# Optimization experiments

Measured on AMD Instinct MI355X. Metric: run time of the kernel, lower is better.

Reference implementation:

```python
import jax, jax.numpy as jnp
import numpy as np

TEMP = 0.05  # contrastive temperature (ContrastiveLoss.temp)
N, D = 8192, 128


def setup_inputs() -> dict:
    key = jax.random.key(0)
    k1, k2 = jax.random.split(key)
    x = jax.random.normal(k1, (N, D), dtype=jnp.float32)
    # Binary positive-pair label matrix; diagonal forced to 1 so every row
    # has at least one positive (positive_pair_nums > 0).
    y = (jax.random.uniform(k2, (N, N)) < 0.05).astype(jnp.float32)
    y = jnp.maximum(y, jnp.eye(N, dtype=jnp.float32))
    return {"x": x, "y": y}


def reference(x, y):
    # similarity(): L2-normalize rows, cosine matmul, exp(cos / temp)
    x_norm = x / jnp.linalg.norm(x, axis=1, keepdims=True)        # [N, D]
    cos_sim = jnp.exp(jnp.matmul(x_norm, x_norm.T) / TEMP)        # [N, N]

    positive_pair_nums = jnp.sum(y, axis=-1)                      # [N]
    neg_y = 1.0 - y
    # hard_mode == 'normal': negative mass per anchor
    nl = jnp.sum(cos_sim * neg_y, axis=-1, keepdims=True)         # [N, 1]

    # sm = log(cos_sim / (cos_sim + nl)); average over positives per row
    sm = jnp.log(cos_sim / (cos_sim + nl))                        # [N, N]
    lm = jnp.sum(sm * y, axis=-1) / positive_pair_nums            # [N]
    return -jnp.mean(lm)
```

## Files before the change

kernel.cpp:

```cpp
#include <hip/hip_runtime.h>
#include <hip/hip_bf16.h>


#define NN 8192

typedef short bf16x8 __attribute__((ext_vector_type(8)));
typedef float f32x4 __attribute__((ext_vector_type(4)));
typedef unsigned long long u64;
typedef unsigned int u32;

__device__ inline unsigned short f32_to_bf16_rne(float f) {
    unsigned u = __float_as_uint(f);
    unsigned r = 0x7FFFu + ((u >> 16) & 1u);
    return (unsigned short)((u + r) >> 16);
}

__global__ __launch_bounds__(256) void prep_kernel(
    const float* __restrict__ x, const float* __restrict__ y,
    unsigned short* __restrict__ xn, u64* __restrict__ bits,
    float* __restrict__ Pp) {
    const int t = threadIdx.x;
    const int w = t >> 6, l = t & 63;
    if (blockIdx.x < 2048) {
        const int row = blockIdx.x * 4 + w;
        float2 v = reinterpret_cast<const float2*>(x)[row * 64 + l];
        float ss = v.x * v.x + v.y * v.y;
#pragma unroll
        for (int m = 1; m < 64; m <<= 1) ss += __shfl_xor(ss, m);
        float rn = 1.0f / sqrtf(ss);
        ushort2 st;
        st.x = f32_to_bf16_rne(v.x * rn);
        st.y = f32_to_bf16_rne(v.y * rn);
        reinterpret_cast<ushort2*>(xn)[row * 64 + l] = st;
    } else {
        const int r = (blockIdx.x - 2048) * 4 + w;
        const float4* yr =
            reinterpret_cast<const float4*>(y + (size_t)r * NN);
        u64* br = bits + (size_t)r * 128;
        int pc = 0;
#pragma unroll 4
        for (int g = 0; g < 32; ++g) {
            float4 v = yr[g * 64 + l];
            u64 m0 = __ballot(v.x != 0.0f);
            u64 m1 = __ballot(v.y != 0.0f);
            u64 m2 = __ballot(v.z != 0.0f);
            u64 m3 = __ballot(v.w != 0.0f);
            pc += __popcll(m0) + __popcll(m1) + __popcll(m2) + __popcll(m3);
            if (l == 0) {
                br[g * 4 + 0] = m0;
                br[g * 4 + 1] = m1;
                br[g * 4 + 2] = m2;
                br[g * 4 + 3] = m3;
            }
        }
        if (l == 0) Pp[r] = (float)pc;
    }
}

template <bool DIAG>
__device__ __forceinline__ void epilogue(
    const f32x4 (&acc)[4][2], const u32 (&W0)[4], const u32 (&W1)[4],
    int shbase, int wM, int wN, int lm16, int lh, int l,
    float* __restrict__ Lb) {
#pragma unroll
    for (int qq = 0; qq < 2; ++qq) {
        float T = 0.0f, A = 0.0f, Y = 0.0f;
        const int rl = wN * 32 + qq * 16 + lm16;
#pragma unroll
        for (int p = 0; p < 4; ++p) {
            const int cl = wM * 64 + p * 16 + lh * 4;
#pragma unroll
            for (int j = 0; j < 4; ++j) {
                float s = 20.0f * acc[p][qq][j];
                float e = __expf(s);
                u32 word = qq ? W1[j] : W0[j];
                u32 bit = (word >> (shbase + p * 4)) & 1u;
                if (DIAG) {
                    if (cl + j == rl) {
                        e = 0.0f;
                        bit = 0u;
                    }
                }
                T += e;
                A += bit ? s : 0.0f;
                Y += bit ? e : 0.0f;
            }
        }
        T += __shfl_xor(T, 16); T += __shfl_xor(T, 32);
        A += __shfl_xor(A, 16); A += __shfl_xor(A, 32);
        Y += __shfl_xor(Y, 16); Y += __shfl_xor(Y, 32);
        if (l < 16) {
            const int r = wN * 32 + qq * 16 + l;
            Lb[(wM * 3 + 0) * 128 + r] = T;
            Lb[(wM * 3 + 1) * 128 + r] = A;
            Lb[(wM * 3 + 2) * 128 + r] = Y;
        }
    }
}

__global__ __launch_bounds__(512, 4) void contrast_main_kernel(
    const unsigned short* __restrict__ xn, const u64* __restrict__ bits,
    float* __restrict__ PtT, float* __restrict__ PtA,
    float* __restrict__ PtY) {
    __shared__ __align__(1024) char lds[68608];
    float* Lb = reinterpret_cast<float*>(lds + 65536);

    const int bid = blockIdx.x;
    const int swz = (bid & 7) * 512 + (bid >> 3);
    const int cb = swz & 63, rb = swz >> 6;
    const int t = threadIdx.x;
    const int w = t >> 6, l = t & 63;
    const int wM = w & 1, wN = w >> 1;
    const int lm16 = l & 15, lh = l >> 4;

    const int g4 = (cb >> 1) * 4;
    const int rbase = rb * 128 + wN * 32;
    u64 B0[4], B1[4];
    {
        const u64* bp0 = bits + (size_t)(rbase + lm16) * 128 + g4;
        const u64* bp1 = bits + (size_t)(rbase + 16 + lm16) * 128 + g4;
        ulonglong2 a0 = *reinterpret_cast<const ulonglong2*>(bp0);
        ulonglong2 a1 = *reinterpret_cast<const ulonglong2*>(bp0 + 2);
        ulonglong2 c0 = *reinterpret_cast<const ulonglong2*>(bp1);
        ulonglong2 c1 = *reinterpret_cast<const ulonglong2*>(bp1 + 2);
        B0[0] = a0.x; B0[1] = a0.y; B0[2] = a1.x; B0[3] = a1.y;
        B1[0] = c0.x; B1[1] = c0.y; B1[2] = c1.x; B1[3] = c1.y;
    }
    const int base = (cb & 1) * 32 + wM * 16;
    const bool hi = base >= 32;
    u32 W0[4], W1[4];
#pragma unroll
    for (int e = 0; e < 4; ++e) {
        W0[e] = hi ? (u32)(B0[e] >> 32) : (u32)B0[e];
        W1[e] = hi ? (u32)(B1[e] >> 32) : (u32)B1[e];
    }
    const int shbase = (base & 31) + lh;

    {
        const char* xb = reinterpret_cast<const char*>(xn);
        const char* srcA = xb + (size_t)cb * 32768;
        const char* srcB = xb + (size_t)rb * 32768;
#pragma unroll
        for (int i = 0; i < 8; ++i) {
            const int p = i * 8192 + t * 16;
            const int pp = p & 32767;
            const int src = pp ^ (((pp >> 8) & 7) << 4);
            __builtin_amdgcn_global_load_lds(
                (const __attribute__((address_space(1))) void*)(
                    (i < 4 ? srcA : srcB) + src),
                (__attribute__((address_space(3))) void*)(lds + p), 16, 0, 0);
        }
    }
    asm volatile("s_waitcnt vmcnt(0)" ::: "memory");
    __syncthreads();

    f32x4 acc[4][2];
#pragma unroll
    for (int i = 0; i < 4; ++i)
#pragma unroll
        for (int j = 0; j < 2; ++j) {
            f32x4 z = {0.0f, 0.0f, 0.0f, 0.0f};
            acc[i][j] = z;
        }

#pragma unroll
    for (int ks = 0; ks < 4; ++ks) {
        bf16x8 af[4], bfr[2];
#pragma unroll
        for (int p = 0; p < 4; ++p) {
            const int c = wM * 64 + p * 16 + lm16;
            const int v = c * 256 + ks * 64 + lh * 16;
            af[p] = *reinterpret_cast<const bf16x8*>(lds + (v ^ ((c & 7) << 4)));
        }
#pragma unroll
        for (int qq = 0; qq < 2; ++qq) {
            const int r = wN * 32 + qq * 16 + lm16;
            const int v = r * 256 + ks * 64 + lh * 16;
            bfr[qq] = *reinterpret_cast<const bf16x8*>(
                lds + 32768 + (v ^ ((r & 7) << 4)));
        }
#pragma unroll
        for (int p = 0; p < 4; ++p)
#pragma unroll
            for (int qq = 0; qq < 2; ++qq)
                acc[p][qq] = __builtin_amdgcn_mfma_f32_16x16x32_bf16(
                    af[p], bfr[qq], acc[p][qq], 0, 0, 0);
    }

    if (rb == cb)
        epilogue<true>(acc, W0, W1, shbase, wM, wN, lm16, lh, l, Lb);
    else
        epilogue<false>(acc, W0, W1, shbase, wM, wN, lm16, lh, l, Lb);
    __syncthreads();

    if (t < 128) {
        const size_t o = (size_t)cb * NN + rb * 128 + t;
        PtT[o] = Lb[0 * 128 + t] + Lb[3 * 128 + t];
        PtA[o] = Lb[1 * 128 + t] + Lb[4 * 128 + t];
        PtY[o] = Lb[2 * 128 + t] + Lb[5 * 128 + t];
    }
}

__global__ __launch_bounds__(256) void finalize_kernel(
    const float* __restrict__ PtT, const float* __restrict__ PtA,
    const float* __restrict__ PtY, const float* __restrict__ Pp,
    float* __restrict__ out) {
    const int t = threadIdx.x;
    const int r = blockIdx.x * 256 + t;
    float T = 0.0f, A = 0.0f, Y = 0.0f;
#pragma unroll 8
    for (int cb = 0; cb < 64; ++cb) {
        T += PtT[(size_t)cb * NN + r];
        A += PtA[(size_t)cb * NN + r];
        Y += PtY[(size_t)cb * NN + r];
    }
    const float P = Pp[r];
    const float nl = T - Y;
    const float lm =
        (A - (P - 1.0f) * logf(nl) - log1pf(nl * 2.0611536e-9f)) / P;

    __shared__ float red[256];
    red[t] = lm;
    __syncthreads();
    for (int k = 128; k > 0; k >>= 1) {
        if (t < k) red[t] += red[t + k];
        __syncthreads();
    }
    if (t == 0) atomicAdd(out, -red[0] * (1.0f / (float)NN));
}

extern "C" void kernel_launch(void* const* d_in, const int* in_sizes, int n_in,
                              void* d_out, int out_size, void* d_ws,
                              size_t ws_size, hipStream_t stream) {
    const float* x = (const float*)d_in[0];
    const float* y = (const float*)d_in[1];

    char* ws = (char*)d_ws;
    unsigned short* xn = (unsigned short*)ws;
    u64* bits = (u64*)(ws + (2ull << 20));
    float* PtT = (float*)(ws + (10ull << 20));
    float* PtA = (float*)(ws + (12ull << 20));
    float* PtY = (float*)(ws + (14ull << 20));
    float* Pp = (float*)(ws + (16ull << 20));

    hipMemsetAsync(d_out, 0, sizeof(float), stream);
    prep_kernel<<<4096, 256, 0, stream>>>(x, y, xn, bits, Pp);
    contrast_main_kernel<<<4096, 512, 0, stream>>>(xn, bits, PtT, PtA, PtY);
    finalize_kernel<<<NN / 256, 256, 0, stream>>>(PtT, PtA, PtY, Pp,
                                                  (float*)d_out);
}
```

Baseline: 410.9 us.

## Shrink main kernel tile to 64x64 with 256 threads and drop LDS reduction

Cuts the Gram-matrix tile from 128x128 (512 threads, 8 waves) to 64x64 (256 threads, 4 waves), quadrupling the grid to 16384 blocks and halving LDS per block. Each wave now owns a whole 16-row strip, so partial sums go straight to global memory and the cross-wave LDS reduction and its second barrier are removed. In exchange the partial-sum buffers double to 128 column blocks, finalize reads twice as much, and operand reuse per loaded byte falls. Also raises the unroll factor of the bit-packing loop in prep.

New measurement: 426.4 us. 3.8% more time.

```diff
diff --git a/kernel.cpp b/kernel.cpp
--- a/kernel.cpp
+++ b/kernel.cpp
@@ -38,7 +38,7 @@
             reinterpret_cast<const float4*>(y + (size_t)r * NN);
         u64* br = bits + (size_t)r * 128;
         int pc = 0;
-#pragma unroll 4
+#pragma unroll 8
         for (int g = 0; g < 32; ++g) {
             float4 v = yr[g * 64 + l];
             u64 m0 = __ballot(v.x != 0.0f);
@@ -59,146 +59,118 @@
 
 template <bool DIAG>
 __device__ __forceinline__ void epilogue(
-    const f32x4 (&acc)[4][2], const u32 (&W0)[4], const u32 (&W1)[4],
-    int shbase, int wM, int wN, int lm16, int lh, int l,
-    float* __restrict__ Lb) {
-#pragma unroll
-    for (int qq = 0; qq < 2; ++qq) {
-        float T = 0.0f, A = 0.0f, Y = 0.0f;
-        const int rl = wN * 32 + qq * 16 + lm16;
-#pragma unroll
-        for (int p = 0; p < 4; ++p) {
-            const int cl = wM * 64 + p * 16 + lh * 4;
-#pragma unroll
-            for (int j = 0; j < 4; ++j) {
-                float s = 20.0f * acc[p][qq][j];
-                float e = __expf(s);
-                u32 word = qq ? W1[j] : W0[j];
-                u32 bit = (word >> (shbase + p * 4)) & 1u;
-                if (DIAG) {
-                    if (cl + j == rl) {
-                        e = 0.0f;
-                        bit = 0u;
-                    }
+    const f32x4 (&acc)[4], const u32 (&W)[4], int shbase, int w, int lm16,
+    int lh, int l, int rb, int cb, float* __restrict__ PtT,
+    float* __restrict__ PtA, float* __restrict__ PtY) {
+    float T = 0.0f, A = 0.0f, Y = 0.0f;
+    const int rl = w * 16 + lm16;
+#pragma unroll
+    for (int p = 0; p < 4; ++p) {
+#pragma unroll
+        for (int j = 0; j < 4; ++j) {
+            float s = 20.0f * acc[p][j];
+            float e = __expf(s);
+            u32 bit = (W[j] >> (shbase + p * 4)) & 1u;
+            if (DIAG) {
+                if (p * 16 + lh * 4 + j == rl) {
+                    e = 0.0f;
+                    bit = 0u;
                 }
-                T += e;
-                A += bit ? s : 0.0f;
-                Y += bit ? e : 0.0f;
             }
-        }
-        T += __shfl_xor(T, 16); T += __shfl_xor(T, 32);
-        A += __shfl_xor(A, 16); A += __shfl_xor(A, 32);
-        Y += __shfl_xor(Y, 16); Y += __shfl_xor(Y, 32);
-        if (l < 16) {
-            const int r = wN * 32 + qq * 16 + l;
-            Lb[(wM * 3 + 0) * 128 + r] = T;
-            Lb[(wM * 3 + 1) * 128 + r] = A;
-            Lb[(wM * 3 + 2) * 128 + r] = Y;
-        }
-    }
-}
-
-__global__ __launch_bounds__(512, 4) void contrast_main_kernel(
+            T += e;
+            A += bit ? s : 0.0f;
+            Y += bit ? e : 0.0f;
+        }
+    }
+    T += __shfl_xor(T, 16); T += __shfl_xor(T, 32);
+    A += __shfl_xor(A, 16); A += __shfl_xor(A, 32);
+    Y += __shfl_xor(Y, 16); Y += __shfl_xor(Y, 32);
+    if (l < 16) {
+        const size_t o = (size_t)cb * NN + rb * 64 + w * 16 + l;
+        PtT[o] = T;
+        PtA[o] = A;
+        PtY[o] = Y;
+    }
+}
+
+__global__ __launch_bounds__(256, 4) void contrast_main_kernel(
     const unsigned short* __restrict__ xn, const u64* __restrict__ bits,
     float* __restrict__ PtT, float* __restrict__ PtA,
     float* __restrict__ PtY) {
-    __shared__ __align__(1024) char lds[68608];
-    float* Lb = reinterpret_cast<float*>(lds + 65536);
+    __shared__ __align__(1024) char lds[32768];
 
     const int bid = blockIdx.x;
-    const int swz = (bid & 7) * 512 + (bid >> 3);
-    const int cb = swz & 63, rb = swz >> 6;
+    const int swz = (bid & 7) * 2048 + (bid >> 3);
+    const int cb = swz & 127, rb = swz >> 7;
     const int t = threadIdx.x;
     const int w = t >> 6, l = t & 63;
-    const int wM = w & 1, wN = w >> 1;
     const int lm16 = l & 15, lh = l >> 4;
 
-    const int g4 = (cb >> 1) * 4;
-    const int rbase = rb * 128 + wN * 32;
-    u64 B0[4], B1[4];
-    {
-        const u64* bp0 = bits + (size_t)(rbase + lm16) * 128 + g4;
-        const u64* bp1 = bits + (size_t)(rbase + 16 + lm16) * 128 + g4;
-        ulonglong2 a0 = *reinterpret_cast<const ulonglong2*>(bp0);
-        ulonglong2 a1 = *reinterpret_cast<const ulonglong2*>(bp0 + 2);
-        ulonglong2 c0 = *reinterpret_cast<const ulonglong2*>(bp1);
-        ulonglong2 c1 = *reinterpret_cast<const ulonglong2*>(bp1 + 2);
-        B0[0] = a0.x; B0[1] = a0.y; B0[2] = a1.x; B0[3] = a1.y;
-        B1[0] = c0.x; B1[1] = c0.y; B1[2] = c1.x; B1[3] = c1.y;
-    }
-    const int base = (cb & 1) * 32 + wM * 16;
-    const bool hi = base >= 32;
-    u32 W0[4], W1[4];
-#pragma unroll
-    for (int e = 0; e < 4; ++e) {
-        W0[e] = hi ? (u32)(B0[e] >> 32) : (u32)B0[e];
-        W1[e] = hi ? (u32)(B1[e] >> 32) : (u32)B1[e];
-    }
-    const int shbase = (base & 31) + lh;
+    const u64* bp =
+        bits + (size_t)(rb * 64 + w * 16 + lm16) * 128 + (cb >> 2) * 4;
+    ulonglong2 b01 = *reinterpret_cast<const ulonglong2*>(bp);
+    ulonglong2 b23 = *reinterpret_cast<const ulonglong2*>(bp + 2);
 
     {
         const char* xb = reinterpret_cast<const char*>(xn);
-        const char* srcA = xb + (size_t)cb * 32768;
-        const char* srcB = xb + (size_t)rb * 32768;
+        const char* srcC = xb + (size_t)cb * 16384;
+        const char* srcR = xb + (size_t)rb * 16384;
 #pragma unroll
         for (int i = 0; i < 8; ++i) {
-            const int p = i * 8192 + t * 16;
-            const int pp = p & 32767;
-            const int src = pp ^ (((pp >> 8) & 7) << 4);
+            const int p = (i & 3) * 4096 + t * 16;
+            const int src = p ^ (((p >> 8) & 7) << 4);
             __builtin_amdgcn_global_load_lds(
                 (const __attribute__((address_space(1))) void*)(
-                    (i < 4 ? srcA : srcB) + src),
-                (__attribute__((address_space(3))) void*)(lds + p), 16, 0, 0);
-        }
-    }
+                    (i < 4 ? srcC : srcR) + src),
+                (__attribute__((address_space(3))) void*)(
+                    lds + (i < 4 ? 0 : 16384) + p),
+                16, 0, 0);
+        }
+    }
+
+    const bool hi = (cb & 3) >= 2;
+    u32 W[4];
+    W[0] = hi ? (u32)(b01.x >> 32) : (u32)b01.x;
+    W[1] = hi ? (u32)(b01.y >> 32) : (u32)b01.y;
+    W[2] = hi ? (u32)(b23.x >> 32) : (u32)b23.x;
+    W[3] = hi ? (u32)(b23.y >> 32) : (u32)b23.y;
+    const int shbase = (cb & 1) * 16 + lh;
+
     asm volatile("s_waitcnt vmcnt(0)" ::: "memory");
     __syncthreads();
 
-    f32x4 acc[4][2];
-#pragma unroll
-    for (int i = 0; i < 4; ++i)
-#pragma unroll
-        for (int j = 0; j < 2; ++j) {
-            f32x4 z = {0.0f, 0.0f, 0.0f, 0.0f};
-            acc[i][j] = z;
-        }
+    f32x4 acc[4];
+#pragma unroll
+    for (int i = 0; i < 4; ++i) {
+        f32x4 z = {0.0f, 0.0f, 0.0f, 0.0f};
+        acc[i] = z;
+    }
 
 #pragma unroll
     for (int ks = 0; ks < 4; ++ks) {
-        bf16x8 af[4], bfr[2];
+        bf16x8 af[4], bfr;
 #pragma unroll
         for (int p = 0; p < 4; ++p) {
-            const int c = wM * 64 + p * 16 + lm16;
+            const int c = p * 16 + lm16;
             const int v = c * 256 + ks * 64 + lh * 16;
             af[p] = *reinterpret_cast<const bf16x8*>(lds + (v ^ ((c & 7) << 4)));
         }
-#pragma unroll
-        for (int qq = 0; qq < 2; ++qq) {
-            const int r = wN * 32 + qq * 16 + lm16;
+        {
+            const int r = w * 16 + lm16;
             const int v = r * 256 + ks * 64 + lh * 16;
-            bfr[qq] = *reinterpret_cast<const bf16x8*>(
-                lds + 32768 + (v ^ ((r & 7) << 4)));
+            bfr = *reinterpret_cast<const bf16x8*>(
+                lds + 16384 + (v ^ ((r & 7) << 4)));
         }
 #pragma unroll
         for (int p = 0; p < 4; ++p)
-#pragma unroll
-            for (int qq = 0; qq < 2; ++qq)
-                acc[p][qq] = __builtin_amdgcn_mfma_f32_16x16x32_bf16(
-                    af[p], bfr[qq], acc[p][qq], 0, 0, 0);
+            acc[p] = __builtin_amdgcn_mfma_f32_16x16x32_bf16(af[p], bfr,
+                                                             acc[p], 0, 0, 0);
     }
 
     if (rb == cb)
-        epilogue<true>(acc, W0, W1, shbase, wM, wN, lm16, lh, l, Lb);
+        epilogue<true>(acc, W, shbase, w, lm16, lh, l, rb, cb, PtT, PtA, PtY);
     else
-        epilogue<false>(acc, W0, W1, shbase, wM, wN, lm16, lh, l, Lb);
-    __syncthreads();
-
-    if (t < 128) {
-        const size_t o = (size_t)cb * NN + rb * 128 + t;
-        PtT[o] = Lb[0 * 128 + t] + Lb[3 * 128 + t];
-        PtA[o] = Lb[1 * 128 + t] + Lb[4 * 128 + t];
-        PtY[o] = Lb[2 * 128 + t] + Lb[5 * 128 + t];
-    }
+        epilogue<false>(acc, W, shbase, w, lm16, lh, l, rb, cb, PtT, PtA, PtY);
 }
 
 __global__ __launch_bounds__(256) void finalize_kernel(
@@ -209,7 +181,7 @@
     const int r = blockIdx.x * 256 + t;
     float T = 0.0f, A = 0.0f, Y = 0.0f;
 #pragma unroll 8
-    for (int cb = 0; cb < 64; ++cb) {
+    for (int cb = 0; cb < 128; ++cb) {
         T += PtT[(size_t)cb * NN + r];
         A += PtA[(size_t)cb * NN + r];
         Y += PtY[(size_t)cb * NN + r];
@@ -239,13 +211,13 @@
     unsigned short* xn = (unsigned short*)ws;
     u64* bits = (u64*)(ws + (2ull << 20));
     float* PtT = (float*)(ws + (10ull << 20));
-    float* PtA = (float*)(ws + (12ull << 20));
-    float* PtY = (float*)(ws + (14ull << 20));
-    float* Pp = (float*)(ws + (16ull << 20));
+    float* PtA = (float*)(ws + (14ull << 20));
+    float* PtY = (float*)(ws + (18ull << 20));
+    float* Pp = (float*)(ws + (22ull << 20));
 
     hipMemsetAsync(d_out, 0, sizeof(float), stream);
     prep_kernel<<<4096, 256, 0, stream>>>(x, y, xn, bits, Pp);
-    contrast_main_kernel<<<4096, 512, 0, stream>>>(xn, bits, PtT, PtA, PtY);
+    contrast_main_kernel<<<16384, 256, 0, stream>>>(xn, bits, PtT, PtA, PtY);
     finalize_kernel<<<NN / 256, 256, 0, stream>>>(PtT, PtA, PtY, Pp,
                                                   (float*)d_out);
 }
```
